# Kernel tuning notes

Measured on AMD Instinct MI355X. Metric: run time of the kernel, lower is better.

Reference implementation:

```python
import jax, jax.numpy as jnp
import numpy as np

BATCH = 512          # bs_large + bs_small
COMBINED_BS = 320    # bs_large + bs_small // (r_large // r_small)
R = 64               # r_large
K = 4096             # hidden dim, fixed in the TIR kernel
N_ADAPT = 80         # combined adapters


def setup_inputs() -> dict:
    key = jax.random.key(0)
    k1, k2, k3, k4 = jax.random.split(key, 4)
    x = jax.random.normal(k1, (BATCH, 1, K), dtype=jnp.float32)
    xids = jax.random.randint(k2, (COMBINED_BS * R,), 0, BATCH, dtype=jnp.int32)
    wids = jax.random.randint(k3, (COMBINED_BS,), 0, N_ADAPT, dtype=jnp.int32)
    A = jax.random.normal(k4, (N_ADAPT, K, R), dtype=jnp.float32) * 0.02
    return {"x": x, "xids": xids, "wids": wids, "A": A}


def reference(x, xids, wids, A):
    # out[c, 0, r] = sum_k x[xids[c*R + r], 0, k] * A[wids[c], k, r]
    C = wids.shape[0]
    r = A.shape[2]
    tok = xids.reshape(C, r)          # per-output-element token ids
    xg = x[tok, 0, :]                 # (C, R, K) gathered activations
    Ag = A[wids]                      # (C, K, R) gathered adapters
    out = jnp.einsum('crk,ckr->cr', xg, Ag)
    return out[:, None, :]            # (C, 1, R)
```

## Files before the change

kernel.cpp:

```cpp
#include <hip/hip_runtime.h>
#include <stdint.h>

namespace {
constexpr int BATCH  = 512;
constexpr int CBS    = 320;
constexpr int R      = 64;
constexpr int K      = 4096;
constexpr int NADAPT = 80;
constexpr int GRP    = 4;
constexpr int NGRP   = CBS / GRP;
constexpr int SPLIT  = 16;
constexpr int KS     = K / SPLIT;
constexpr int TK     = 32;
constexpr int NTILE  = KS / TK;
constexpr int NT     = 256;

constexpr size_t WS_X_OFF  = 4096;
constexpr size_t WS_NEEDED = WS_X_OFF + (size_t)BATCH * K * 2;

__device__ inline uint16_t f2bf(float f) {
    uint32_t u = __float_as_uint(f);
    u += 0x7fffu + ((u >> 16) & 1u);
    return (uint16_t)(u >> 16);
}
__device__ inline float bflo(uint32_t u) { return __uint_as_float(u << 16); }
__device__ inline float bfhi(uint32_t u) { return __uint_as_float(u & 0xffff0000u); }
}

__global__ __launch_bounds__(256)
void prep(const float* __restrict__ x, uint16_t* __restrict__ xb,
          const int* __restrict__ wids, int* __restrict__ perm,
          float* __restrict__ out, int out_size)
{
    const int bid = blockIdx.x;
    const int t   = threadIdx.x;
    if (bid == 0) {
        __shared__ int hist[NADAPT];
        __shared__ int offs[NADAPT];
        if (t < NADAPT) hist[t] = 0;
        __syncthreads();
        for (int c = t; c < CBS; c += 256) atomicAdd(&hist[wids[c]], 1);
        __syncthreads();
        if (t == 0) {
            int run = 0;
            for (int i = 0; i < NADAPT; ++i) { offs[i] = run; run += hist[i]; }
        }
        __syncthreads();
        for (int c = t; c < CBS; c += 256) {
            const int pos = atomicAdd(&offs[wids[c]], 1);
            perm[pos] = c;
        }
    } else if (bid <= BATCH * K / 1024) {
        const int i = (bid - 1) * 256 + t;
        const float4 v = ((const float4*)x)[i];
        ushort4 o;
        o.x = f2bf(v.x); o.y = f2bf(v.y); o.z = f2bf(v.z); o.w = f2bf(v.w);
        ((ushort4*)xb)[i] = o;
    } else {
        const int i4 = (bid - (1 + BATCH * K / 1024)) * 256 + t;
        const int e  = i4 * 4;
        if (e + 3 < out_size) {
            ((float4*)out)[i4] = make_float4(0.f, 0.f, 0.f, 0.f);
        } else {
            for (int q = e; q < out_size; ++q) out[q] = 0.f;
        }
    }
}

__global__ __launch_bounds__(NT, 4)
void lora_main(const int* __restrict__ xids,
               const int* __restrict__ wids,
               const float* __restrict__ A,
               const uint16_t* __restrict__ xb,
               const int* __restrict__ perm,
               float* __restrict__ out)
{
    __shared__ __align__(16) uint32_t xs[2][GRP * 1024];
    __shared__ float red[4 * GRP * 64];

    const int bid = blockIdx.x;
    const int g   = bid >> 4;
    const int s   = bid & 15;
    const int t   = threadIdx.x;
    const int wv  = t >> 6;
    const int r   = t & 63;

    const int c0 = perm[GRP * g + 0], c1 = perm[GRP * g + 1],
              c2 = perm[GRP * g + 2], c3 = perm[GRP * g + 3];
    const int w0 = wids[c0], w1 = wids[c1], w2 = wids[c2], w3 = wids[c3];

    const int cc = wv;
    const int ccombo = (wv == 0) ? c0 : (wv == 1) ? c1 : (wv == 2) ? c2 : c3;
    const uint16_t* __restrict__ xrow =
        xb + (size_t)xids[ccombo * R + r] * K + s * KS;

    const size_t koff = (size_t)(s * KS) * R + r;
    const float* __restrict__ Ab0 = A + (size_t)w0 * (K * R) + koff;
    const float* __restrict__ Ab1 = A + (size_t)w1 * (K * R) + koff;
    const float* __restrict__ Ab2 = A + (size_t)w2 * (K * R) + koff;
    const float* __restrict__ Ab3 = A + (size_t)w3 * (K * R) + koff;
    const bool uniform = (w0 == w3);

    float acc0 = 0.f, acc1 = 0.f, acc2 = 0.f, acc3 = 0.f;

#define DOT8(ACC, V, AP) do {                                              \
        ACC = fmaf(bflo((V).x), (AP)[0], ACC);                             \
        ACC = fmaf(bfhi((V).x), (AP)[1], ACC);                             \
        ACC = fmaf(bflo((V).y), (AP)[2], ACC);                             \
        ACC = fmaf(bfhi((V).y), (AP)[3], ACC);                             \
        ACC = fmaf(bflo((V).z), (AP)[4], ACC);                             \
        ACC = fmaf(bfhi((V).z), (AP)[5], ACC);                             \
        ACC = fmaf(bflo((V).w), (AP)[6], ACC);                             \
        ACC = fmaf(bfhi((V).w), (AP)[7], ACC);                             \
    } while (0)

    uint4 p0, p1, p2, p3;
    {
        const uint4* src = (const uint4*)xrow;
        p0 = src[0]; p1 = src[1]; p2 = src[2]; p3 = src[3];
        uint32_t* wb = &xs[0][cc * 1024 + 4 * r];
        *(uint4*)(wb +   0) = p0;
        *(uint4*)(wb + 256) = p1;
        *(uint4*)(wb + 512) = p2;
        *(uint4*)(wb + 768) = p3;
    }

    for (int tile = 0; tile < NTILE; ++tile) {
        if (tile + 1 < NTILE) {
            const uint4* src = (const uint4*)(xrow + (tile + 1) * TK);
            p0 = src[0]; p1 = src[1]; p2 = src[2]; p3 = src[3];
        }
        __syncthreads();

        const uint32_t* __restrict__ B = &xs[tile & 1][wv * 256 + 4 * r];
        const size_t ao = (size_t)(tile * TK + wv * 8) * R;
        const uint4 x0 = *(const uint4*)(B + 0 * 1024);
        const uint4 x1 = *(const uint4*)(B + 1 * 1024);
        const uint4 x2 = *(const uint4*)(B + 2 * 1024);
        const uint4 x3 = *(const uint4*)(B + 3 * 1024);

        if (uniform) {
            const float* At = Ab0 + ao;
            float a[8];
#pragma unroll
            for (int q = 0; q < 8; ++q) a[q] = At[(size_t)q * R];
            DOT8(acc0, x0, a);
            DOT8(acc1, x1, a);
            DOT8(acc2, x2, a);
            DOT8(acc3, x3, a);
        } else {
            {
                const float* At = Ab0 + ao; float a[8];
#pragma unroll
                for (int q = 0; q < 8; ++q) a[q] = At[(size_t)q * R];
                DOT8(acc0, x0, a);
            }
            {
                const float* At = Ab1 + ao; float a[8];
#pragma unroll
                for (int q = 0; q < 8; ++q) a[q] = At[(size_t)q * R];
                DOT8(acc1, x1, a);
            }
            {
                const float* At = Ab2 + ao; float a[8];
#pragma unroll
                for (int q = 0; q < 8; ++q) a[q] = At[(size_t)q * R];
                DOT8(acc2, x2, a);
            }
            {
                const float* At = Ab3 + ao; float a[8];
#pragma unroll
                for (int q = 0; q < 8; ++q) a[q] = At[(size_t)q * R];
                DOT8(acc3, x3, a);
            }
        }

        if (tile + 1 < NTILE) {
            uint32_t* wb = &xs[(tile + 1) & 1][cc * 1024 + 4 * r];
            *(uint4*)(wb +   0) = p0;
            *(uint4*)(wb + 256) = p1;
            *(uint4*)(wb + 512) = p2;
            *(uint4*)(wb + 768) = p3;
        }
    }
#undef DOT8

    red[wv * 256 +   0 + r] = acc0;
    red[wv * 256 +  64 + r] = acc1;
    red[wv * 256 + 128 + r] = acc2;
    red[wv * 256 + 192 + r] = acc3;
    __syncthreads();
    const float sum = red[0 * 256 + wv * 64 + r] + red[1 * 256 + wv * 64 + r] +
                      red[2 * 256 + wv * 64 + r] + red[3 * 256 + wv * 64 + r];
    atomicAdd(&out[ccombo * R + r], sum);
}

__global__ __launch_bounds__(NT)
void lora_fallback(const float* __restrict__ x,
                   const int*   __restrict__ xids,
                   const int*   __restrict__ wids,
                   const float* __restrict__ A,
                   float*       __restrict__ out)
{
    constexpr int FKS = 512, FTK = 64, FNT_TILES = 8, FNW = 4;
    __shared__ float xsf[FTK * R];
    __shared__ float red[FNW * R];
    const int bid  = blockIdx.x;
    const int c    = bid >> 3;
    const int s    = bid & 7;
    const int t    = threadIdx.x;
    const int wave = t >> 6;
    const int lane = t & 63;
    const int r4   = lane & 15;
    const int kq   = lane >> 4;
    const int wid  = wids[c];
    const float* __restrict__ Aw = A + (size_t)wid * (K * R);
    const int rw  = t >> 2;
    const int jq  = t & 3;
    const int tok = xids[c * R + rw];
    const float* __restrict__ xrow = x + (size_t)tok * K + s * FKS + jq * 16;
    float4 acc = make_float4(0.f, 0.f, 0.f, 0.f);
    float4 pv[4];
    {
        const float4* src = (const float4*)xrow;
#pragma unroll
        for (int ii = 0; ii < 4; ++ii) pv[ii] = src[ii];
    }
    for (int tile = 0; tile < FNT_TILES; ++tile) {
#pragma unroll
        for (int ii = 0; ii < 4; ++ii) {
            const int kk = jq * 16 + ii * 4;
            xsf[(kk + 0) * R + rw] = pv[ii].x;
            xsf[(kk + 1) * R + rw] = pv[ii].y;
            xsf[(kk + 2) * R + rw] = pv[ii].z;
            xsf[(kk + 3) * R + rw] = pv[ii].w;
        }
        __syncthreads();
        if (tile + 1 < FNT_TILES) {
            const float4* src = (const float4*)(xrow + (tile + 1) * FTK);
#pragma unroll
            for (int ii = 0; ii < 4; ++ii) pv[ii] = src[ii];
        }
        const int kw = wave * 16 + kq;
        const float* __restrict__ Ap =
            Aw + (size_t)(s * FKS + tile * FTK + kw) * R + 4 * r4;
#pragma unroll
        for (int i = 0; i < 4; ++i) {
            float4 av = *(const float4*)(Ap + (size_t)(4 * i) * R);
            float4 xv = *(const float4*)(&xsf[(kw + 4 * i) * R + 4 * r4]);
            acc.x = fmaf(xv.x, av.x, acc.x);
            acc.y = fmaf(xv.y, av.y, acc.y);
            acc.z = fmaf(xv.z, av.z, acc.z);
            acc.w = fmaf(xv.w, av.w, acc.w);
        }
        __syncthreads();
    }
#pragma unroll
    for (int m = 16; m < 64; m <<= 1) {
        acc.x += __shfl_xor(acc.x, m, 64);
        acc.y += __shfl_xor(acc.y, m, 64);
        acc.z += __shfl_xor(acc.z, m, 64);
        acc.w += __shfl_xor(acc.w, m, 64);
    }
    if (kq == 0) {
        float* rd = &red[wave * R + 4 * r4];
        rd[0] = acc.x; rd[1] = acc.y; rd[2] = acc.z; rd[3] = acc.w;
    }
    __syncthreads();
    if (wave == 0) {
        float sum = red[lane] + red[R + lane] + red[2 * R + lane] + red[3 * R + lane];
        atomicAdd(&out[c * R + lane], sum);
    }
}

extern "C" void kernel_launch(void* const* d_in, const int* in_sizes, int n_in,
                              void* d_out, int out_size, void* d_ws, size_t ws_size,
                              hipStream_t stream)
{
    (void)in_sizes; (void)n_in;
    const float* x    = (const float*)d_in[0];
    const int*   xids = (const int*)d_in[1];
    const int*   wids = (const int*)d_in[2];
    const float* A    = (const float*)d_in[3];
    float* out        = (float*)d_out;

    if (ws_size >= WS_NEEDED) {
        int*      perm = (int*)d_ws;
        uint16_t* xbw  = (uint16_t*)((char*)d_ws + WS_X_OFF);
        const int ncvt = BATCH * K / 1024;
        const int nz   = (out_size + 1023) / 1024;
        hipLaunchKernelGGL(prep, dim3(1 + ncvt + nz), dim3(256), 0, stream,
                           x, xbw, wids, perm, out, out_size);
        hipLaunchKernelGGL(lora_main, dim3(NGRP * SPLIT), dim3(NT), 0, stream,
                           xids, wids, A, xbw, perm, out);
    } else {
        hipMemsetAsync(out, 0, (size_t)out_size * sizeof(float), stream);
        hipLaunchKernelGGL(lora_fallback, dim3(CBS * 8), dim3(NT), 0, stream,
                           x, xids, wids, A, out);
    }
}
```

Measured before the change: 160.0 us.

## Group combos per adapter with padding and software-pipeline main loop manually

The prep kernel now builds groups of up to four combos that all share one adapter, padding incomplete groups with -1, and writes the group count to a header. Every block therefore reads a single A stream, and the per-combo branches for mixed adapters go away. The main loop is fully unrolled through a templated body. It prefetches x two tiles ahead and A one tile ahead, with explicit vmcnt/lgkmcnt waits, sched barriers and raw s_barrier. The cost is a larger fixed grid (140 groups) with early exits, padded idle waves, and fragile hand-tuned wait counts.

```diff
diff --git a/kernel.cpp b/kernel.cpp
--- a/kernel.cpp
+++ b/kernel.cpp
@@ -8,15 +8,16 @@
 constexpr int K      = 4096;
 constexpr int NADAPT = 80;
 constexpr int GRP    = 4;
-constexpr int NGRP   = CBS / GRP;
+constexpr int NGMAX  = 140;
 constexpr int SPLIT  = 16;
 constexpr int KS     = K / SPLIT;
 constexpr int TK     = 32;
 constexpr int NTILE  = KS / TK;
 constexpr int NT     = 256;
 
-constexpr size_t WS_X_OFF  = 4096;
-constexpr size_t WS_NEEDED = WS_X_OFF + (size_t)BATCH * K * 2;
+constexpr size_t WS_GRP_OFF = 64;
+constexpr size_t WS_X_OFF   = 4096;
+constexpr size_t WS_NEEDED  = WS_X_OFF + (size_t)BATCH * K * 2;
 
 __device__ inline uint16_t f2bf(float f) {
     uint32_t u = __float_as_uint(f);
@@ -25,30 +26,107 @@
 }
 __device__ inline float bflo(uint32_t u) { return __uint_as_float(u << 16); }
 __device__ inline float bfhi(uint32_t u) { return __uint_as_float(u & 0xffff0000u); }
+
+__device__ __forceinline__ void dot8(float& acc, const uint4 v, const float (&a)[8]) {
+    acc = fmaf(bflo(v.x), a[0], acc);
+    acc = fmaf(bfhi(v.x), a[1], acc);
+    acc = fmaf(bflo(v.y), a[2], acc);
+    acc = fmaf(bfhi(v.y), a[3], acc);
+    acc = fmaf(bflo(v.z), a[4], acc);
+    acc = fmaf(bfhi(v.z), a[5], acc);
+    acc = fmaf(bflo(v.w), a[6], acc);
+    acc = fmaf(bfhi(v.w), a[7], acc);
+}
+
+#define WAITL() asm volatile("s_waitcnt lgkmcnt(0)" ::: "memory")
+#define SCHED0() __builtin_amdgcn_sched_barrier(0)
+#define SBAR()  __builtin_amdgcn_s_barrier()
+
+template<int T, bool IX2, bool IA1, bool WRT, int WN>
+__device__ __forceinline__ void body(
+    uint32_t* __restrict__ xs_base,
+    const uint16_t* __restrict__ xrow,
+    const float* __restrict__ Ab,
+    int wv, int r,
+    uint4 (&pxN)[4], const uint4 (&pxW)[4],
+    float (&aN)[8], const float (&aC)[8],
+    float& acc0, float& acc1, float& acc2, float& acc3)
+{
+    const uint32_t* Bp = xs_base + (T & 1) * 4096 + wv * 256 + 4 * r;
+    const uint4 xv0 = *(const uint4*)(Bp + 0 * 1024);
+    const uint4 xv1 = *(const uint4*)(Bp + 1 * 1024);
+    const uint4 xv2 = *(const uint4*)(Bp + 2 * 1024);
+    const uint4 xv3 = *(const uint4*)(Bp + 3 * 1024);
+    if constexpr (IX2) {
+        const uint4* s2 = (const uint4*)(xrow + (T + 2) * TK);
+        pxN[0] = s2[0]; pxN[1] = s2[1]; pxN[2] = s2[2]; pxN[3] = s2[3];
+    }
+    if constexpr (IA1) {
+#pragma unroll
+        for (int q = 0; q < 8; ++q)
+            aN[q] = Ab[((size_t)((T + 1) * TK) + wv * 8 + q) * R];
+    }
+    asm volatile("s_waitcnt vmcnt(%0)" :: "i"(WN) : "memory");
+    WAITL();
+    SCHED0();
+    dot8(acc0, xv0, aC);
+    dot8(acc1, xv1, aC);
+    dot8(acc2, xv2, aC);
+    dot8(acc3, xv3, aC);
+    if constexpr (WRT) {
+        uint32_t* wb = xs_base + ((T + 1) & 1) * 4096 + wv * 1024 + 4 * r;
+        *(uint4*)(wb +   0) = pxW[0];
+        *(uint4*)(wb + 256) = pxW[1];
+        *(uint4*)(wb + 512) = pxW[2];
+        *(uint4*)(wb + 768) = pxW[3];
+        WAITL(); SCHED0();
+        SBAR();
+        SCHED0();
+    }
+}
 }
 
 __global__ __launch_bounds__(256)
 void prep(const float* __restrict__ x, uint16_t* __restrict__ xb,
-          const int* __restrict__ wids, int* __restrict__ perm,
-          float* __restrict__ out, int out_size)
+          const int* __restrict__ wids, int* __restrict__ hdr,
+          int* __restrict__ grp, float* __restrict__ out, int out_size)
 {
     const int bid = blockIdx.x;
     const int t   = threadIdx.x;
     if (bid == 0) {
         __shared__ int hist[NADAPT];
         __shared__ int offs[NADAPT];
+        __shared__ int gbase[NADAPT + 1];
+        __shared__ int sperm[CBS];
         if (t < NADAPT) hist[t] = 0;
         __syncthreads();
         for (int c = t; c < CBS; c += 256) atomicAdd(&hist[wids[c]], 1);
         __syncthreads();
         if (t == 0) {
-            int run = 0;
-            for (int i = 0; i < NADAPT; ++i) { offs[i] = run; run += hist[i]; }
+            int run = 0, grun = 0;
+            for (int i = 0; i < NADAPT; ++i) {
+                offs[i]  = run;  run  += hist[i];
+                gbase[i] = grun; grun += (hist[i] + GRP - 1) / GRP;
+            }
+            gbase[NADAPT] = grun;
+            hdr[0] = grun;
         }
         __syncthreads();
         for (int c = t; c < CBS; c += 256) {
             const int pos = atomicAdd(&offs[wids[c]], 1);
-            perm[pos] = c;
+            sperm[pos] = c;
+        }
+        __syncthreads();
+        for (int w = t; w < NADAPT; w += 256) {
+            const int cnt   = hist[w];
+            const int start = offs[w] - cnt;
+            const int gb    = gbase[w];
+            for (int i = 0; i < cnt; i += GRP) {
+                const int gi = gb + i / GRP;
+#pragma unroll
+                for (int j = 0; j < GRP; ++j)
+                    grp[GRP * gi + j] = (i + j < cnt) ? sperm[start + i + j] : -1;
+            }
         }
     } else if (bid <= BATCH * K / 1024) {
         const int i = (bid - 1) * 256 + t;
@@ -72,7 +150,8 @@
                const int* __restrict__ wids,
                const float* __restrict__ A,
                const uint16_t* __restrict__ xb,
-               const int* __restrict__ perm,
+               const int* __restrict__ hdr,
+               const int* __restrict__ grp,
                float* __restrict__ out)
 {
     __shared__ __align__(16) uint32_t xs[2][GRP * 1024];
@@ -81,109 +160,54 @@
     const int bid = blockIdx.x;
     const int g   = bid >> 4;
     const int s   = bid & 15;
-    const int t   = threadIdx.x;
-    const int wv  = t >> 6;
-    const int r   = t & 63;
-
-    const int c0 = perm[GRP * g + 0], c1 = perm[GRP * g + 1],
-              c2 = perm[GRP * g + 2], c3 = perm[GRP * g + 3];
-    const int w0 = wids[c0], w1 = wids[c1], w2 = wids[c2], w3 = wids[c3];
-
-    const int cc = wv;
-    const int ccombo = (wv == 0) ? c0 : (wv == 1) ? c1 : (wv == 2) ? c2 : c3;
-    const uint16_t* __restrict__ xrow =
-        xb + (size_t)xids[ccombo * R + r] * K + s * KS;
-
-    const size_t koff = (size_t)(s * KS) * R + r;
-    const float* __restrict__ Ab0 = A + (size_t)w0 * (K * R) + koff;
-    const float* __restrict__ Ab1 = A + (size_t)w1 * (K * R) + koff;
-    const float* __restrict__ Ab2 = A + (size_t)w2 * (K * R) + koff;
-    const float* __restrict__ Ab3 = A + (size_t)w3 * (K * R) + koff;
-    const bool uniform = (w0 == w3);
+    if (g >= hdr[0]) return;
+
+    const int t  = threadIdx.x;
+    const int wv = t >> 6;
+    const int r  = t & 63;
+
+    const int* gp = grp + GRP * g;
+    const int gc0 = gp[0], gc1 = gp[1], gc2 = gp[2], gc3 = gp[3];
+    const int myc_raw = (wv == 0) ? gc0 : (wv == 1) ? gc1 : (wv == 2) ? gc2 : gc3;
+    const int myc = (myc_raw >= 0) ? myc_raw : gc0;
+    const int wid = wids[gc0];
+
+    const uint16_t* __restrict__ xrow = xb + (size_t)xids[myc * R + r] * K + s * KS;
+    const float* __restrict__ Ab = A + (size_t)wid * (K * R) + (size_t)(s * KS) * R + r;
 
     float acc0 = 0.f, acc1 = 0.f, acc2 = 0.f, acc3 = 0.f;
-
-#define DOT8(ACC, V, AP) do {                                              \
-        ACC = fmaf(bflo((V).x), (AP)[0], ACC);                             \
-        ACC = fmaf(bfhi((V).x), (AP)[1], ACC);                             \
-        ACC = fmaf(bflo((V).y), (AP)[2], ACC);                             \
-        ACC = fmaf(bfhi((V).y), (AP)[3], ACC);                             \
-        ACC = fmaf(bflo((V).z), (AP)[4], ACC);                             \
-        ACC = fmaf(bfhi((V).z), (AP)[5], ACC);                             \
-        ACC = fmaf(bflo((V).w), (AP)[6], ACC);                             \
-        ACC = fmaf(bfhi((V).w), (AP)[7], ACC);                             \
-    } while (0)
-
-    uint4 p0, p1, p2, p3;
+    uint4 pxA[4], pxB[4];
+    float aA[8], aB[8];
+
     {
-        const uint4* src = (const uint4*)xrow;
-        p0 = src[0]; p1 = src[1]; p2 = src[2]; p3 = src[3];
-        uint32_t* wb = &xs[0][cc * 1024 + 4 * r];
-        *(uint4*)(wb +   0) = p0;
-        *(uint4*)(wb + 256) = p1;
-        *(uint4*)(wb + 512) = p2;
-        *(uint4*)(wb + 768) = p3;
-    }
-
-    for (int tile = 0; tile < NTILE; ++tile) {
-        if (tile + 1 < NTILE) {
-            const uint4* src = (const uint4*)(xrow + (tile + 1) * TK);
-            p0 = src[0]; p1 = src[1]; p2 = src[2]; p3 = src[3];
-        }
-        __syncthreads();
-
-        const uint32_t* __restrict__ B = &xs[tile & 1][wv * 256 + 4 * r];
-        const size_t ao = (size_t)(tile * TK + wv * 8) * R;
-        const uint4 x0 = *(const uint4*)(B + 0 * 1024);
-        const uint4 x1 = *(const uint4*)(B + 1 * 1024);
-        const uint4 x2 = *(const uint4*)(B + 2 * 1024);
-        const uint4 x3 = *(const uint4*)(B + 3 * 1024);
-
-        if (uniform) {
-            const float* At = Ab0 + ao;
-            float a[8];
-#pragma unroll
-            for (int q = 0; q < 8; ++q) a[q] = At[(size_t)q * R];
-            DOT8(acc0, x0, a);
-            DOT8(acc1, x1, a);
-            DOT8(acc2, x2, a);
-            DOT8(acc3, x3, a);
-        } else {
-            {
-                const float* At = Ab0 + ao; float a[8];
-#pragma unroll
-                for (int q = 0; q < 8; ++q) a[q] = At[(size_t)q * R];
-                DOT8(acc0, x0, a);
-            }
-            {
-                const float* At = Ab1 + ao; float a[8];
-#pragma unroll
-                for (int q = 0; q < 8; ++q) a[q] = At[(size_t)q * R];
-                DOT8(acc1, x1, a);
-            }
-            {
-                const float* At = Ab2 + ao; float a[8];
-#pragma unroll
-                for (int q = 0; q < 8; ++q) a[q] = At[(size_t)q * R];
-                DOT8(acc2, x2, a);
-            }
-            {
-                const float* At = Ab3 + ao; float a[8];
-#pragma unroll
-                for (int q = 0; q < 8; ++q) a[q] = At[(size_t)q * R];
-                DOT8(acc3, x3, a);
-            }
-        }
-
-        if (tile + 1 < NTILE) {
-            uint32_t* wb = &xs[(tile + 1) & 1][cc * 1024 + 4 * r];
-            *(uint4*)(wb +   0) = p0;
-            *(uint4*)(wb + 256) = p1;
-            *(uint4*)(wb + 512) = p2;
-            *(uint4*)(wb + 768) = p3;
-        }
-    }
-#undef DOT8
+        const uint4* s0p = (const uint4*)xrow;
+        pxA[0] = s0p[0]; pxA[1] = s0p[1]; pxA[2] = s0p[2]; pxA[3] = s0p[3];
+        SCHED0();
+        const uint4* s1p = (const uint4*)(xrow + TK);
+        pxB[0] = s1p[0]; pxB[1] = s1p[1]; pxB[2] = s1p[2]; pxB[3] = s1p[3];
+        SCHED0();
+#pragma unroll
+        for (int q = 0; q < 8; ++q) aA[q] = Ab[(size_t)(wv * 8 + q) * R];
+        asm volatile("s_waitcnt vmcnt(12)" ::: "memory");
+        uint32_t* wb = &xs[0][wv * 1024 + 4 * r];
+        *(uint4*)(wb +   0) = pxA[0];
+        *(uint4*)(wb + 256) = pxA[1];
+        *(uint4*)(wb + 512) = pxA[2];
+        *(uint4*)(wb + 768) = pxA[3];
+        WAITL(); SCHED0();
+        SBAR();
+        SCHED0();
+    }
+
+    uint32_t* xsb = &xs[0][0];
+    body<0, true,  true,  true, 12>(xsb, xrow, Ab, wv, r, pxA, pxB, aB, aA, acc0, acc1, acc2, acc3);
+    body<1, true,  true,  true, 12>(xsb, xrow, Ab, wv, r, pxB, pxA, aA, aB, acc0, acc1, acc2, acc3);
+    body<2, true,  true,  true, 12>(xsb, xrow, Ab, wv, r, pxA, pxB, aB, aA, acc0, acc1, acc2, acc3);
+    body<3, true,  true,  true, 12>(xsb, xrow, Ab, wv, r, pxB, pxA, aA, aB, acc0, acc1, acc2, acc3);
+    body<4, true,  true,  true, 12>(xsb, xrow, Ab, wv, r, pxA, pxB, aB, aA, acc0, acc1, acc2, acc3);
+    body<5, true,  true,  true, 12>(xsb, xrow, Ab, wv, r, pxB, pxA, aA, aB, acc0, acc1, acc2, acc3);
+    body<6, false, true,  true,  8>(xsb, xrow, Ab, wv, r, pxA, pxB, aB, aA, acc0, acc1, acc2, acc3);
+    body<7, false, false, false, 0>(xsb, xrow, Ab, wv, r, pxB, pxA, aA, aB, acc0, acc1, acc2, acc3);
 
     red[wv * 256 +   0 + r] = acc0;
     red[wv * 256 +  64 + r] = acc1;
@@ -192,7 +216,8 @@
     __syncthreads();
     const float sum = red[0 * 256 + wv * 64 + r] + red[1 * 256 + wv * 64 + r] +
                       red[2 * 256 + wv * 64 + r] + red[3 * 256 + wv * 64 + r];
-    atomicAdd(&out[ccombo * R + r], sum);
+    if (myc_raw >= 0)
+        atomicAdd(&out[myc_raw * R + r], sum);
 }
 
 __global__ __launch_bounds__(NT)
@@ -285,14 +310,15 @@
     float* out        = (float*)d_out;
 
     if (ws_size >= WS_NEEDED) {
-        int*      perm = (int*)d_ws;
-        uint16_t* xbw  = (uint16_t*)((char*)d_ws + WS_X_OFF);
+        int*      hdr = (int*)d_ws;
+        int*      grp = (int*)((char*)d_ws + WS_GRP_OFF);
+        uint16_t* xbw = (uint16_t*)((char*)d_ws + WS_X_OFF);
         const int ncvt = BATCH * K / 1024;
         const int nz   = (out_size + 1023) / 1024;
         hipLaunchKernelGGL(prep, dim3(1 + ncvt + nz), dim3(256), 0, stream,
-                           x, xbw, wids, perm, out, out_size);
-        hipLaunchKernelGGL(lora_main, dim3(NGRP * SPLIT), dim3(NT), 0, stream,
-                           xids, wids, A, xbw, perm, out);
+                           x, xbw, wids, hdr, grp, out, out_size);
+        hipLaunchKernelGGL(lora_main, dim3(NGMAX * SPLIT), dim3(NT), 0, stream,
+                           xids, wids, A, xbw, hdr, grp, out);
     } else {
         hipMemsetAsync(out, 0, (size_t)out_size * sizeof(float), stream);
         hipLaunchKernelGGL(lora_fallback, dim3(CBS * 8), dim3(NT), 0, stream,
```

Result: no change. 158.1 us (-1.2%).
